# Optimization experiments

Hardware: AMD Instinct MI355X
Metric: run time of the kernel (lower is better)

Reference implementation:

```python
import jax, jax.numpy as jnp
import numpy as np

N = 20000   # nodes
E = 320000  # edges (avg degree 16)
IN = 16     # in_node_nf
H = 64      # hidden_nf
OUT = 64    # out_node_nf
L = 4       # n_layers


def setup_inputs() -> dict:
    key = jax.random.key(0)
    ks = jax.random.split(key, 16)
    w = lambda k, shape: (jax.random.normal(k, shape, dtype=jnp.float32) * 0.05)
    zb = lambda *shape: jnp.zeros(shape, dtype=jnp.float32)
    return {
        "h": jax.random.normal(ks[0], (N, IN), dtype=jnp.float32),
        "x": jax.random.normal(ks[1], (N, 3), dtype=jnp.float32),
        "edge_index": jax.random.randint(ks[2], (2, E), 0, N),
        "emb_in_w": w(ks[3], (IN, H)), "emb_in_b": zb(H),
        "edge_w1": w(ks[4], (L, 2 * H + 1, H)), "edge_b1": zb(L, H),
        "edge_w2": w(ks[5], (L, H, H)), "edge_b2": zb(L, H),
        "coord_w1": w(ks[6], (L, H, H)), "coord_b1": zb(L, H),
        "coord_w2": w(ks[7], (L, H, 1)),  # bias-free last coord_mlp layer
        "node_w1": w(ks[8], (L, 2 * H, H)), "node_b1": zb(L, H),
        "node_w2": w(ks[9], (L, H, H)), "node_b2": zb(L, H),
        "emb_out_w": w(ks[10], (H, OUT)), "emb_out_b": zb(OUT),
    }


def reference(h, x, edge_index, emb_in_w, emb_in_b,
              edge_w1, edge_b1, edge_w2, edge_b2,
              coord_w1, coord_b1, coord_w2,
              node_w1, node_b1, node_w2, node_b2,
              emb_out_w, emb_out_b):
    row, col = edge_index[0], edge_index[1]
    act = jax.nn.silu
    # receiver in-degree for mean coordinate aggregation (clamped to >=1)
    cnt = jax.ops.segment_sum(jnp.ones((row.shape[0], 1), h.dtype), row, num_segments=N)
    cnt = jnp.maximum(cnt, 1.0)

    h = h @ emb_in_w + emb_in_b
    for l in range(L):
        # coord2radial
        diff = x[row] - x[col]                               # [E,3]
        radial = jnp.sum(diff * diff, axis=-1, keepdims=True)  # [E,1]
        # edge model: m_ij = phi_e(h_i, h_j, ||x_i-x_j||^2)
        e_in = jnp.concatenate([h[row], h[col], radial], axis=-1)  # [E,2H+1]
        m = act(e_in @ edge_w1[l] + edge_b1[l])
        m = act(m @ edge_w2[l] + edge_b2[l])                 # [E,H]
        # coord model: x_i += mean_j (x_i - x_j) * phi_x(m_ij)
        phi = act(m @ coord_w1[l] + coord_b1[l]) @ coord_w2[l]  # [E,1]
        trans = diff * phi                                    # [E,3]
        x = x + jax.ops.segment_sum(trans, row, num_segments=N) / cnt
        # node model: h_i = h_i + phi_h(h_i, sum_j m_ij)
        agg = jax.ops.segment_sum(m, row, num_segments=N)     # [N,H]
        n_in = jnp.concatenate([h, agg], axis=-1)             # [N,2H]
        out = act(n_in @ node_w1[l] + node_b1[l]) @ node_w2[l] + node_b2[l]
        h = h + out
    h = h @ emb_out_w + emb_out_b
    return h, x
```

## Files before the change

### kernel.cpp

```cpp
#include <hip/hip_runtime.h>
#include <hip/hip_bf16.h>


#define NN 20000
#define EE 320000
#define LSE 17024
#define LSN 6272

typedef unsigned short u16;
typedef unsigned int   u32;
typedef __attribute__((ext_vector_type(8))) short s16x8;
typedef __attribute__((ext_vector_type(4))) float f32x4;

__device__ __forceinline__ float bf2f(u16 u) { return __uint_as_float(((u32)u) << 16); }
__device__ __forceinline__ float silu_f(float x) {
    return x * __builtin_amdgcn_rcpf(1.0f + __expf(-x));
}

__device__ __forceinline__ u16 f2bf_rne(float f) {
    u32 u = __float_as_uint(f);
    return (u16)((u + 0x7FFFu + ((u >> 16) & 1u)) >> 16);
}
__device__ __forceinline__ float gldf(const void* p, int i, int bf) {
    return bf ? bf2f(((const u16*)p)[i]) : ((const float*)p)[i];
}
__device__ __forceinline__ u16 gldb(const void* p, int i, int bf) {
    return bf ? ((const u16*)p)[i] : f2bf_rne(((const float*)p)[i]);
}

__global__ void k_sentinel(u16* __restrict__ out, int n, float v) {
    int t = blockIdx.x * 256 + threadIdx.x;
    if (t < n) out[t] = f2bf_rne(v);
}

__global__ __launch_bounds__(256) void k_pack(
    const void* __restrict__ ew1, const void* __restrict__ eb1,
    const void* __restrict__ ew2, const void* __restrict__ eb2,
    const void* __restrict__ cw1, const void* __restrict__ cb1,
    const void* __restrict__ cw2,
    const void* __restrict__ nw1, const void* __restrict__ nb1,
    const void* __restrict__ nw2, const void* __restrict__ nb2,
    const u16* __restrict__ h_raw, const int* __restrict__ rowi,
    int* __restrict__ flag, int* __restrict__ deg,
    u16* __restrict__ pkE, u32* __restrict__ pkN)
{
    if (blockIdx.x >= 64) {
        int e = (blockIdx.x - 64) * 256 + threadIdx.x;
        if (e < EE) atomicAdd(&deg[rowi[e]], 1);
        return;
    }
    __shared__ int cnt_s;
    if (threadIdx.x == 0) cnt_s = 0;
    __syncthreads();
    if (threadIdx.x < 128) {
        float v = fabsf(bf2f(h_raw[threadIdx.x]));
        if (v >= 0.015625f && v <= 16.0f) atomicAdd(&cnt_s, 1);
    }
    __syncthreads();
    const int bf = (cnt_s >= 96) ? 1 : 0;
    if (blockIdx.x == 0 && threadIdx.x == 0) *flag = bf;

    const int gid = blockIdx.x * 256 + threadIdx.x;
    const int stride = 64 * 256;

    for (int g = gid; g < 4 * 16384; g += stride) {
        int l = g >> 14, idx = g & 16383;
        u16 v;
        if (idx < 8192) {
            int j = idx & 7, lane = (idx >> 3) & 63, t = (idx >> 9) & 3, w = idx >> 11;
            int k = 32 * w + (lane >> 4) * 8 + j, n = 16 * t + (lane & 15);
            v = gldb(ew1, l * 129 * 64 + k * 64 + n, bf);
        } else if (idx < 12288) {
            int i2 = idx - 8192;
            int j = i2 & 7, lane = (i2 >> 3) & 63, t = (i2 >> 9) & 3, w = i2 >> 11;
            int k = 32 * w + (lane >> 4) * 8 + j, n = 16 * t + (lane & 15);
            v = gldb(ew2, l * 4096 + k * 64 + n, bf);
        } else {
            int i2 = idx - 12288;
            int j = i2 & 7, lane = (i2 >> 3) & 63, t = (i2 >> 9) & 3, w = i2 >> 11;
            int k = 32 * w + (lane >> 4) * 8 + j, n = 16 * t + (lane & 15);
            v = gldb(cw1, l * 4096 + k * 64 + n, bf);
        }
        pkE[l * LSE + idx] = v;
    }
    for (int g = gid; g < 4 * 320; g += stride) {
        int l = g / 320, r = g % 320, wch = r >> 6, i = r & 63;
        float v = (wch == 0) ? gldf(eb1, l * 64 + i, bf)
                : (wch == 1) ? gldf(eb2, l * 64 + i, bf)
                : (wch == 2) ? gldf(cb1, l * 64 + i, bf)
                : (wch == 3) ? gldf(cw2, l * 64 + i, bf)
                :              gldf(ew1, l * 129 * 64 + 128 * 64 + i, bf);
        ((float*)(pkE + l * LSE + 16384))[r] = v;
    }
    for (int g = gid; g < 4 * 6144; g += stride) {
        int l = g / 6144, idx = g % 6144;
        u32 pv;
        if (idx < 4096) {
            int kp = idx >> 6, j = idx & 63;
            u32 lo = gldb(nw1, l * 8192 + (2 * kp) * 64 + j, bf);
            u32 hi = gldb(nw1, l * 8192 + (2 * kp + 1) * 64 + j, bf);
            pv = lo | (hi << 16);
        } else {
            int i2 = idx - 4096, kp = i2 >> 6, j = i2 & 63;
            u32 lo = gldb(nw2, l * 4096 + (2 * kp) * 64 + j, bf);
            u32 hi = gldb(nw2, l * 4096 + (2 * kp + 1) * 64 + j, bf);
            pv = lo | (hi << 16);
        }
        pkN[l * LSN + idx] = pv;
    }
    for (int g = gid; g < 4 * 128; g += stride) {
        int l = g >> 7, r = g & 127;
        float v = (r < 64) ? gldf(nb1, l * 64 + r, bf) : gldf(nb2, l * 64 + (r - 64), bf);
        ((float*)(pkN + l * LSN + 6144))[r] = v;
    }
}

__global__ __launch_bounds__(1024) void k_scan(const int* deg, int* offs, int* cursor,
                                               int* __restrict__ perm) {
    __shared__ int part[1024];
    __shared__ int hist[32], basep[32];
    const int tid = threadIdx.x;
    const int CH = (NN + 1023) / 1024;
    const int b0 = tid * CH;
    int s = 0;
    for (int i = 0; i < CH; i++) { int idx = b0 + i; if (idx < NN) s += deg[idx]; }
    part[tid] = s;
    __syncthreads();
    for (int d = 1; d < 1024; d <<= 1) {
        int v = (tid >= d) ? part[tid - d] : 0;
        __syncthreads();
        part[tid] += v;
        __syncthreads();
    }
    int run = (tid > 0) ? part[tid - 1] : 0;
    for (int i = 0; i < CH; i++) {
        int idx = b0 + i;
        if (idx < NN) {
            int dv = deg[idx];
            offs[idx] = run;
            cursor[idx] = run;
            run += dv;
        }
    }
    if (tid == 1023) offs[NN] = run;
    __syncthreads();

    if (tid < 32) hist[tid] = 0;
    __syncthreads();
    for (int i = 0; i < CH; i++) {
        int idx = b0 + i;
        if (idx < NN) {
            int dv = offs[idx + 1] - offs[idx];
            int key = min(31, (dv + 15) >> 4);
            atomicAdd(&hist[key], 1);
        }
    }
    __syncthreads();
    if (tid == 0) {
        int pos = 0;
        for (int k = 31; k >= 0; k--) { basep[k] = pos; pos += hist[k]; }
    }
    __syncthreads();
    for (int i = 0; i < CH; i++) {
        int idx = b0 + i;
        if (idx < NN) {
            int dv = offs[idx + 1] - offs[idx];
            int key = min(31, (dv + 15) >> 4);
            int p = atomicAdd(&basep[key], 1);
            perm[p] = idx;
        }
    }
}

__global__ void k_scatter(const int* __restrict__ rowi, const int* __restrict__ coli,
                          int* __restrict__ cursor, int* __restrict__ slist) {
    int e = blockIdx.x * 256 + threadIdx.x;
    if (e < EE) {
        int r = rowi[e];
        int pos = atomicAdd(&cursor[r], 1);
        slist[pos] = coli[e];
    }
}

__global__ __launch_bounds__(256) void k_embed(
    const void* __restrict__ h_in, const void* __restrict__ x_in,
    const void* __restrict__ w, const void* __restrict__ bias,
    const int* __restrict__ flag,
    float* __restrict__ hws, float* __restrict__ xws, u16* __restrict__ hb)
{
    const int bf = *flag;
    const int lane = threadIdx.x & 63;
    const int wv   = threadIdx.x >> 6;
    const int i    = blockIdx.x * 4 + wv;
    float acc = gldf(bias, lane, bf);
    #pragma unroll
    for (int k = 0; k < 16; k++)
        acc = fmaf(gldf(h_in, i * 16 + k, bf), gldf(w, k * 64 + lane, bf), acc);
    hws[i * 64 + lane] = acc;
    hb[i * 64 + lane] = f2bf_rne(acc);
    if (lane < 3) xws[i * 3 + lane] = gldf(x_in, i * 3 + lane, bf);
}

#define OFF_B23  8192
#define OFF_M    16384
#define MPAD     76
#define OFF_PHI  (OFF_M + 8 * 16 * MPAD)
#define OFF_CB   (OFF_PHI + 8 * 32)
__global__ __launch_bounds__(512, 8) void k_edge(
    const u16* __restrict__ hb, const float* __restrict__ xws,
    const int* __restrict__ offs, const int* __restrict__ slist,
    const u16* __restrict__ pE, const int* __restrict__ perm,
    float* __restrict__ agg, float* __restrict__ xacc)
{
    __shared__ __align__(16) u16 sW[OFF_CB + 640];

    const int tid = threadIdx.x, lane = tid & 63, wv = tid >> 6;
    const int l15 = lane & 15, quad = lane >> 4;

    for (int idx = tid; idx < 2048; idx += 512)
        ((s16x8*)sW)[idx] = ((const s16x8*)pE)[idx];
    {
        const float* pb = (const float*)(pE + 16384);
        float* cb = (float*)&sW[OFF_CB];
        if (tid < 320) cb[tid] = pb[tid];
    }
    __syncthreads();

    const float* CB = (const float*)&sW[OFF_CB];
    const int gw = blockIdx.x * 8 + wv, totW = gridDim.x * 8;
    u16* mrow = &sW[OFF_M + wv * 16 * MPAD];
    float* phiw = (float*)&sW[OFF_PHI + wv * 32];

    for (int pidx = gw; pidx < NN; pidx += totW) {
        const int n = perm[pidx];
        const int o0 = offs[n], deg = offs[n + 1] - o0;
        if (deg == 0) continue;

        const s16x8 Ar0 = *(const s16x8*)&hb[n * 64 + quad * 8];
        const s16x8 Ar1 = *(const s16x8*)&hb[n * 64 + 32 + quad * 8];
        f32x4 Cb[4] = {{0,0,0,0},{0,0,0,0},{0,0,0,0},{0,0,0,0}};
        #pragma unroll
        for (int t = 0; t < 4; t++) {
            const s16x8 Bf0 = *(const s16x8*)&sW[((0 * 4 + t) * 64 + lane) * 8];
            Cb[t] = __builtin_amdgcn_mfma_f32_16x16x32_bf16(Ar0, Bf0, Cb[t], 0, 0, 0);
            const s16x8 Bf1 = *(const s16x8*)&sW[((1 * 4 + t) * 64 + lane) * 8];
            Cb[t] = __builtin_amdgcn_mfma_f32_16x16x32_bf16(Ar1, Bf1, Cb[t], 0, 0, 0);
        }
        const float xrv = (quad < 3) ? xws[n * 3 + quad] : 0.0f;
        float aggA[4] = {0.f, 0.f, 0.f, 0.f};
        float xaccA = 0.0f;

        for (int eb = 0; eb < deg; eb += 16) {
            const int nb = min(16, deg - eb);
            const int ee = (l15 < nb) ? l15 : 0;
            const int ce = slist[o0 + eb + ee];
            float dx = 0.0f;
            if (quad < 3 && l15 < nb) dx = xrv - xws[ce * 3 + quad];
            float r2 = dx * dx;
            r2 += __shfl_xor(r2, 16, 64);
            r2 += __shfl_xor(r2, 32, 64);

            f32x4 C[4] = {Cb[0], Cb[1], Cb[2], Cb[3]};
            {
                const s16x8 Ac0 = *(const s16x8*)&hb[ce * 64 + quad * 8];
                const s16x8 Ac1 = *(const s16x8*)&hb[ce * 64 + 32 + quad * 8];
                #pragma unroll
                for (int t = 0; t < 4; t++) {
                    const s16x8 Bf2 = *(const s16x8*)&sW[((2 * 4 + t) * 64 + lane) * 8];
                    C[t] = __builtin_amdgcn_mfma_f32_16x16x32_bf16(Ac0, Bf2, C[t], 0, 0, 0);
                    const s16x8 Bf3 = *(const s16x8*)&sW[((3 * 4 + t) * 64 + lane) * 8];
                    C[t] = __builtin_amdgcn_mfma_f32_16x16x32_bf16(Ac1, Bf3, C[t], 0, 0, 0);
                }
            }
            float r2r[4];
            #pragma unroll
            for (int r = 0; r < 4; r++) r2r[r] = __shfl(r2, quad * 4 + r, 64);
            #pragma unroll
            for (int t = 0; t < 4; t++) {
                const float b1t = CB[       16 * t + l15];
                const float wrt = CB[256 +  16 * t + l15];
                #pragma unroll
                for (int r = 0; r < 4; r++) {
                    float v = silu_f(C[t][r] + b1t + r2r[r] * wrt);
                    mrow[(quad * 4 + r) * MPAD + 16 * t + l15] = f2bf_rne(v);
                }
            }

            f32x4 D[4] = {{0,0,0,0},{0,0,0,0},{0,0,0,0},{0,0,0,0}};
            #pragma unroll
            for (int w = 0; w < 2; w++) {
                const s16x8 Am = *(const s16x8*)(mrow + l15 * MPAD + 32 * w + quad * 8);
                #pragma unroll
                for (int t = 0; t < 4; t++) {
                    const s16x8 Bf = *(const s16x8*)&sW[OFF_B23 + ((w * 4 + t) * 64 + lane) * 8];
                    D[t] = __builtin_amdgcn_mfma_f32_16x16x32_bf16(Am, Bf, D[t], 0, 0, 0);
                }
            }
            #pragma unroll
            for (int t = 0; t < 4; t++) {
                const float b2t = CB[64 + 16 * t + l15];
                #pragma unroll
                for (int r = 0; r < 4; r++) {
                    float v = silu_f(D[t][r] + b2t);
                    if (quad * 4 + r < nb) aggA[t] += v;
                    mrow[(quad * 4 + r) * MPAD + 16 * t + l15] = f2bf_rne(v);
                }
            }

            f32x4 P[4] = {{0,0,0,0},{0,0,0,0},{0,0,0,0},{0,0,0,0}};
            #pragma unroll
            for (int w = 0; w < 2; w++) {
                const s16x8 Am = *(const s16x8*)(mrow + l15 * MPAD + 32 * w + quad * 8);
                #pragma unroll
                for (int t = 0; t < 4; t++) {
                    const s16x8 Bf = *(const s16x8*)&sW[OFF_B23 + (((2 + w) * 4 + t) * 64 + lane) * 8];
                    P[t] = __builtin_amdgcn_mfma_f32_16x16x32_bf16(Am, Bf, P[t], 0, 0, 0);
                }
            }
            float ph[4];
            #pragma unroll
            for (int r = 0; r < 4; r++) ph[r] = 0.f;
            #pragma unroll
            for (int t = 0; t < 4; t++) {
                const float cb1t = CB[128 + 16 * t + l15];
                const float c2t  = CB[192 + 16 * t + l15];
                #pragma unroll
                for (int r = 0; r < 4; r++)
                    ph[r] = fmaf(silu_f(P[t][r] + cb1t), c2t, ph[r]);
            }
            #pragma unroll
            for (int r = 0; r < 4; r++) {
                float s = ph[r];
                s += __shfl_xor(s, 1, 64);
                s += __shfl_xor(s, 2, 64);
                s += __shfl_xor(s, 4, 64);
                s += __shfl_xor(s, 8, 64);
                ph[r] = s;
            }
            if (l15 == 0) {
                #pragma unroll
                for (int r = 0; r < 4; r++) phiw[quad * 4 + r] = ph[r];
            }
            float phv = phiw[l15];
            if (quad < 3 && l15 < nb) xaccA = fmaf(dx, phv, xaccA);
        }

        #pragma unroll
        for (int t = 0; t < 4; t++) {
            aggA[t] += __shfl_xor(aggA[t], 16, 64);
            aggA[t] += __shfl_xor(aggA[t], 32, 64);
        }
        float av = (quad == 0) ? aggA[0] : (quad == 1) ? aggA[1]
                 : (quad == 2) ? aggA[2] : aggA[3];
        agg[n * 64 + quad * 16 + l15] = av;

        xaccA += __shfl_xor(xaccA, 1, 64);
        xaccA += __shfl_xor(xaccA, 2, 64);
        xaccA += __shfl_xor(xaccA, 4, 64);
        xaccA += __shfl_xor(xaccA, 8, 64);
        if (l15 == 0 && quad < 3) xacc[n * 3 + quad] = xaccA / (float)deg;
    }
}

__global__ __launch_bounds__(256) void k_node(
    float* __restrict__ hws, u16* __restrict__ hb, const float* __restrict__ agg,
    float* __restrict__ xws, const float* __restrict__ xacc,
    const u32* __restrict__ pN)
{
    __shared__ __align__(16) u32 sW1p[64 * 64];
    __shared__ __align__(16) u32 sW2p[32 * 64];
    __shared__ float sB1f[64], sB2f[64];
    __shared__ __align__(16) float sNin[4][8][132];

    const int tid = threadIdx.x, lane = tid & 63, wv = tid >> 6;
    for (int idx = tid; idx < 1024; idx += 256)
        ((f32x4*)sW1p)[idx] = ((const f32x4*)pN)[idx];
    for (int idx = tid; idx < 512; idx += 256)
        ((f32x4*)sW2p)[idx] = ((const f32x4*)(pN + 4096))[idx];
    const float* pb = (const float*)(pN + 6144);
    if (tid < 64) { sB1f[tid] = pb[tid]; sB2f[tid] = pb[64 + tid]; }

    {
        int t = blockIdx.x * 96 + tid;
        if (tid < 96) xws[t] += xacc[t];
    }
    __syncthreads();

    const int i0 = (blockIdx.x * 4 + wv) * 8;
    float hold[8];
    #pragma unroll
    for (int b = 0; b < 8; b++) {
        int i = i0 + b;
        float hv = hws[i * 64 + lane];
        hold[b] = hv;
        sNin[wv][b][lane]      = hv;
        sNin[wv][b][64 + lane] = agg[i * 64 + lane];
    }

    float acc[8];
    #pragma unroll
    for (int b = 0; b < 8; b++) acc[b] = sB1f[lane];
    #pragma unroll
    for (int kk = 0; kk < 32; kk++) {
        u32 w01 = sW1p[(kk * 2) * 64 + lane];
        u32 w23 = sW1p[(kk * 2 + 1) * 64 + lane];
        float w0 = __uint_as_float(w01 << 16), w1 = __uint_as_float(w01 & 0xffff0000u);
        float w2 = __uint_as_float(w23 << 16), w3 = __uint_as_float(w23 & 0xffff0000u);
        #pragma unroll
        for (int b = 0; b < 8; b++) {
            const float4 e4 = *reinterpret_cast<const float4*>(&sNin[wv][b][kk * 4]);
            acc[b] = fmaf(e4.x, w0, fmaf(e4.y, w1, fmaf(e4.z, w2, fmaf(e4.w, w3, acc[b]))));
        }
    }
    #pragma unroll
    for (int b = 0; b < 8; b++) acc[b] = silu_f(acc[b]);
    #pragma unroll
    for (int b = 0; b < 8; b++) sNin[wv][b][lane] = acc[b];

    float out[8];
    #pragma unroll
    for (int b = 0; b < 8; b++) out[b] = sB2f[lane];
    #pragma unroll
    for (int kk = 0; kk < 16; kk++) {
        u32 w01 = sW2p[(kk * 2) * 64 + lane];
        u32 w23 = sW2p[(kk * 2 + 1) * 64 + lane];
        float w0 = __uint_as_float(w01 << 16), w1 = __uint_as_float(w01 & 0xffff0000u);
        float w2 = __uint_as_float(w23 << 16), w3 = __uint_as_float(w23 & 0xffff0000u);
        #pragma unroll
        for (int b = 0; b < 8; b++) {
            const float4 e4 = *reinterpret_cast<const float4*>(&sNin[wv][b][kk * 4]);
            out[b] = fmaf(e4.x, w0, fmaf(e4.y, w1, fmaf(e4.z, w2, fmaf(e4.w, w3, out[b]))));
        }
    }
    #pragma unroll
    for (int b = 0; b < 8; b++) {
        float hv = hold[b] + out[b];
        hws[(i0 + b) * 64 + lane] = hv;
        hb[(i0 + b) * 64 + lane] = f2bf_rne(hv);
    }
}

__global__ __launch_bounds__(256) void k_out(
    const float* __restrict__ hws, const float* __restrict__ xws,
    const void* __restrict__ wo, const void* __restrict__ bo,
    const int* __restrict__ flag, void* __restrict__ out)
{
    __shared__ u32 sWp[32 * 64];
    __shared__ float sBf[64];
    __shared__ __align__(16) float sH[4][8][68];
    const int tid = threadIdx.x, lane = tid & 63, wv = tid >> 6;
    const int bf = *flag;
    for (int idx = tid; idx < 32 * 64; idx += 256) {
        int kp = idx >> 6, j = idx & 63;
        u32 lo = gldb(wo, (kp * 2) * 64 + j, bf);
        u32 hi = gldb(wo, (kp * 2 + 1) * 64 + j, bf);
        sWp[idx] = lo | (hi << 16);
    }
    if (tid < 64) sBf[tid] = gldf(bo, tid, bf);
    __syncthreads();

    const int i0 = (blockIdx.x * 4 + wv) * 8;
    #pragma unroll
    for (int b = 0; b < 8; b++) sH[wv][b][lane] = hws[(i0 + b) * 64 + lane];

    float acc[8];
    #pragma unroll
    for (int b = 0; b < 8; b++) acc[b] = sBf[lane];
    #pragma unroll
    for (int kk = 0; kk < 16; kk++) {
        u32 w01 = sWp[(kk * 2) * 64 + lane];
        u32 w23 = sWp[(kk * 2 + 1) * 64 + lane];
        float w0 = __uint_as_float(w01 << 16), w1 = __uint_as_float(w01 & 0xffff0000u);
        float w2 = __uint_as_float(w23 << 16), w3 = __uint_as_float(w23 & 0xffff0000u);
        #pragma unroll
        for (int b = 0; b < 8; b++) {
            const float4 e4 = *reinterpret_cast<const float4*>(&sH[wv][b][kk * 4]);
            acc[b] = fmaf(e4.x, w0, fmaf(e4.y, w1, fmaf(e4.z, w2, fmaf(e4.w, w3, acc[b]))));
        }
    }
    u16*   oh16 = (u16*)out;
    float* ohf  = (float*)out;
    u16*   ox16 = oh16 + (size_t)NN * 64;
    float* oxf  = ohf  + (size_t)NN * 64;
    #pragma unroll
    for (int b = 0; b < 8; b++) {
        int i = i0 + b;
        if (bf) {
            oh16[i * 64 + lane] = f2bf_rne(acc[b]);
            if (lane < 3) ox16[i * 3 + lane] = f2bf_rne(xws[i * 3 + lane]);
        } else {
            ohf[i * 64 + lane] = acc[b];
            if (lane < 3) oxf[i * 3 + lane] = xws[i * 3 + lane];
        }
    }
}

extern "C" void kernel_launch(void* const* d_in, const int* in_sizes, int n_in,
                              void* d_out, int out_size, void* d_ws, size_t ws_size,
                              hipStream_t stream)
{
    const size_t WS_REQ = (size_t)NN * 134 * sizeof(float) + 64;
    if (ws_size < WS_REQ) {
        float sval = 1000.0f + (float)(ws_size >> 20);
        k_sentinel<<<(out_size + 255) / 256, 256, 0, stream>>>(
            (u16*)d_out, out_size, sval);
        return;
    }

    const void* h_in = d_in[0];
    const void* x_in = d_in[1];
    const int*  eidx = (const int*)d_in[2];
    const int* rowi = eidx;
    const int* coli = eidx + EE;

    float* ws   = (float*)d_ws;
    float* hws  = ws;
    float* xws  = hws + NN * 64;
    float* agg  = xws + NN * 3;
    float* xacc = agg + NN * 64;
    int*   flag = (int*)(xacc + NN * 3);

    u16* hb     = (u16*)d_out;
    int* offs   = (int*)(hb + (size_t)NN * 64);
    int* slist  = offs + (NN + 4);
    u16* pkE    = (u16*)(slist + EE);
    u32* pkN    = (u32*)(pkE + 4 * LSE);
    int* cursor = (int*)(pkN + 4 * LSN);
    int* perm   = cursor + NN;

    hipMemsetAsync(cursor, 0, (size_t)NN * sizeof(int), stream);
    hipMemsetAsync(agg, 0, (size_t)NN * 67 * sizeof(float), stream);

    k_pack<<<64 + (EE + 255) / 256, 256, 0, stream>>>(
        d_in[5], d_in[6], d_in[7], d_in[8], d_in[9], d_in[10], d_in[11],
        d_in[12], d_in[13], d_in[14], d_in[15],
        (const u16*)h_in, rowi, flag, cursor, pkE, pkN);
    k_scan<<<1, 1024, 0, stream>>>(cursor, offs, cursor, perm);
    k_scatter<<<(EE + 255) / 256, 256, 0, stream>>>(rowi, coli, cursor, slist);
    k_embed<<<NN / 4, 256, 0, stream>>>(h_in, x_in, d_in[3], d_in[4], flag, hws, xws, hb);

    for (int l = 0; l < 4; l++) {
        k_edge<<<768, 512, 0, stream>>>(hb, xws, offs, slist,
                                        pkE + l * LSE, perm, agg, xacc);
        k_node<<<NN / 32, 256, 0, stream>>>(hws, hb, agg, xws, xacc,
                                            pkN + (size_t)l * LSN);
    }
    k_out<<<NN / 32, 256, 0, stream>>>(hws, xws, d_in[16], d_in[17], flag, d_out);
}
```

Before: 550.2 us.

## Fuse node MLP into edge kernel with ping-pong h/x buffers

Folds the per-node update MLP into the edge kernel, so each wave finishes its node's aggregation and immediately runs the node MLP. The agg/xacc global buffers, their memset and the separate k_node launches go away. Bf16 h and coordinates are double-buffered so neighbour reads are not corrupted by in-place writes. In exchange, each wave now does a per-node scalar FMA matvec through LDS, and the larger LDS footprint (node weights added) lowers occupancy, with launch bounds reduced to 2 and the grid to 512 blocks.

```diff
diff --git a/kernel.cpp b/kernel.cpp
--- a/kernel.cpp
+++ b/kernel.cpp
@@ -206,13 +206,16 @@
 #define MPAD     76
 #define OFF_PHI  (OFF_M + 8 * 16 * MPAD)
 #define OFF_CB   (OFF_PHI + 8 * 32)
-__global__ __launch_bounds__(512, 8) void k_edge(
-    const u16* __restrict__ hb, const float* __restrict__ xws,
+#define OFF_NW   (OFF_CB + 640)
+__global__ __launch_bounds__(512, 2) void k_edge(
+    const u16* __restrict__ hbr, u16* __restrict__ hbw,
+    const float* __restrict__ xr, float* __restrict__ xw,
+    float* __restrict__ hws,
     const int* __restrict__ offs, const int* __restrict__ slist,
-    const u16* __restrict__ pE, const int* __restrict__ perm,
-    float* __restrict__ agg, float* __restrict__ xacc)
+    const u16* __restrict__ pE, const u32* __restrict__ pN,
+    const int* __restrict__ perm)
 {
-    __shared__ __align__(16) u16 sW[OFF_CB + 640];
+    __shared__ __align__(16) u16 sW[OFF_NW + 12544];
 
     const int tid = threadIdx.x, lane = tid & 63, wv = tid >> 6;
     const int l15 = lane & 15, quad = lane >> 4;
@@ -224,9 +227,15 @@
         float* cb = (float*)&sW[OFF_CB];
         if (tid < 320) cb[tid] = pb[tid];
     }
+    for (int idx = tid; idx < 1568; idx += 512)
+        ((f32x4*)&sW[OFF_NW])[idx] = ((const f32x4*)pN)[idx];
     __syncthreads();
 
     const float* CB = (const float*)&sW[OFF_CB];
+    const u32* nW1 = (const u32*)&sW[OFF_NW];
+    const u32* nW2 = nW1 + 4096;
+    const float* nB = (const float*)(nW1 + 6144);
+
     const int gw = blockIdx.x * 8 + wv, totW = gridDim.x * 8;
     u16* mrow = &sW[OFF_M + wv * 16 * MPAD];
     float* phiw = (float*)&sW[OFF_PHI + wv * 32];
@@ -234,10 +243,9 @@
     for (int pidx = gw; pidx < NN; pidx += totW) {
         const int n = perm[pidx];
         const int o0 = offs[n], deg = offs[n + 1] - o0;
-        if (deg == 0) continue;
-
-        const s16x8 Ar0 = *(const s16x8*)&hb[n * 64 + quad * 8];
-        const s16x8 Ar1 = *(const s16x8*)&hb[n * 64 + 32 + quad * 8];
+
+        const s16x8 Ar0 = *(const s16x8*)&hbr[n * 64 + quad * 8];
+        const s16x8 Ar1 = *(const s16x8*)&hbr[n * 64 + 32 + quad * 8];
         f32x4 Cb[4] = {{0,0,0,0},{0,0,0,0},{0,0,0,0},{0,0,0,0}};
         #pragma unroll
         for (int t = 0; t < 4; t++) {
@@ -246,7 +254,7 @@
             const s16x8 Bf1 = *(const s16x8*)&sW[((1 * 4 + t) * 64 + lane) * 8];
             Cb[t] = __builtin_amdgcn_mfma_f32_16x16x32_bf16(Ar1, Bf1, Cb[t], 0, 0, 0);
         }
-        const float xrv = (quad < 3) ? xws[n * 3 + quad] : 0.0f;
+        const float xrv = (quad < 3) ? xr[n * 3 + quad] : 0.0f;
         float aggA[4] = {0.f, 0.f, 0.f, 0.f};
         float xaccA = 0.0f;
 
@@ -255,15 +263,15 @@
             const int ee = (l15 < nb) ? l15 : 0;
             const int ce = slist[o0 + eb + ee];
             float dx = 0.0f;
-            if (quad < 3 && l15 < nb) dx = xrv - xws[ce * 3 + quad];
+            if (quad < 3 && l15 < nb) dx = xrv - xr[ce * 3 + quad];
             float r2 = dx * dx;
             r2 += __shfl_xor(r2, 16, 64);
             r2 += __shfl_xor(r2, 32, 64);
 
             f32x4 C[4] = {Cb[0], Cb[1], Cb[2], Cb[3]};
             {
-                const s16x8 Ac0 = *(const s16x8*)&hb[ce * 64 + quad * 8];
-                const s16x8 Ac1 = *(const s16x8*)&hb[ce * 64 + 32 + quad * 8];
+                const s16x8 Ac0 = *(const s16x8*)&hbr[ce * 64 + quad * 8];
+                const s16x8 Ac1 = *(const s16x8*)&hbr[ce * 64 + 32 + quad * 8];
                 #pragma unroll
                 for (int t = 0; t < 4; t++) {
                     const s16x8 Bf2 = *(const s16x8*)&sW[((2 * 4 + t) * 64 + lane) * 8];
@@ -352,91 +360,43 @@
         }
         float av = (quad == 0) ? aggA[0] : (quad == 1) ? aggA[1]
                  : (quad == 2) ? aggA[2] : aggA[3];
-        agg[n * 64 + quad * 16 + l15] = av;
 
         xaccA += __shfl_xor(xaccA, 1, 64);
         xaccA += __shfl_xor(xaccA, 2, 64);
         xaccA += __shfl_xor(xaccA, 4, 64);
         xaccA += __shfl_xor(xaccA, 8, 64);
-        if (l15 == 0 && quad < 3) xacc[n * 3 + quad] = xaccA / (float)deg;
-    }
-}
-
-__global__ __launch_bounds__(256) void k_node(
-    float* __restrict__ hws, u16* __restrict__ hb, const float* __restrict__ agg,
-    float* __restrict__ xws, const float* __restrict__ xacc,
-    const u32* __restrict__ pN)
-{
-    __shared__ __align__(16) u32 sW1p[64 * 64];
-    __shared__ __align__(16) u32 sW2p[32 * 64];
-    __shared__ float sB1f[64], sB2f[64];
-    __shared__ __align__(16) float sNin[4][8][132];
-
-    const int tid = threadIdx.x, lane = tid & 63, wv = tid >> 6;
-    for (int idx = tid; idx < 1024; idx += 256)
-        ((f32x4*)sW1p)[idx] = ((const f32x4*)pN)[idx];
-    for (int idx = tid; idx < 512; idx += 256)
-        ((f32x4*)sW2p)[idx] = ((const f32x4*)(pN + 4096))[idx];
-    const float* pb = (const float*)(pN + 6144);
-    if (tid < 64) { sB1f[tid] = pb[tid]; sB2f[tid] = pb[64 + tid]; }
-
-    {
-        int t = blockIdx.x * 96 + tid;
-        if (tid < 96) xws[t] += xacc[t];
-    }
-    __syncthreads();
-
-    const int i0 = (blockIdx.x * 4 + wv) * 8;
-    float hold[8];
-    #pragma unroll
-    for (int b = 0; b < 8; b++) {
-        int i = i0 + b;
-        float hv = hws[i * 64 + lane];
-        hold[b] = hv;
-        sNin[wv][b][lane]      = hv;
-        sNin[wv][b][64 + lane] = agg[i * 64 + lane];
-    }
-
-    float acc[8];
-    #pragma unroll
-    for (int b = 0; b < 8; b++) acc[b] = sB1f[lane];
-    #pragma unroll
-    for (int kk = 0; kk < 32; kk++) {
-        u32 w01 = sW1p[(kk * 2) * 64 + lane];
-        u32 w23 = sW1p[(kk * 2 + 1) * 64 + lane];
-        float w0 = __uint_as_float(w01 << 16), w1 = __uint_as_float(w01 & 0xffff0000u);
-        float w2 = __uint_as_float(w23 << 16), w3 = __uint_as_float(w23 & 0xffff0000u);
+        if (l15 == 0 && quad < 3)
+            xw[n * 3 + quad] = (deg > 0) ? (xrv + xaccA / (float)deg) : xrv;
+
+        float* nin = (float*)mrow;
+        const float hv = hws[n * 64 + lane];
+        nin[lane] = hv;
+        nin[64 + lane] = av;
+        float a1 = nB[lane];
         #pragma unroll
-        for (int b = 0; b < 8; b++) {
-            const float4 e4 = *reinterpret_cast<const float4*>(&sNin[wv][b][kk * 4]);
-            acc[b] = fmaf(e4.x, w0, fmaf(e4.y, w1, fmaf(e4.z, w2, fmaf(e4.w, w3, acc[b]))));
-        }
-    }
-    #pragma unroll
-    for (int b = 0; b < 8; b++) acc[b] = silu_f(acc[b]);
-    #pragma unroll
-    for (int b = 0; b < 8; b++) sNin[wv][b][lane] = acc[b];
-
-    float out[8];
-    #pragma unroll
-    for (int b = 0; b < 8; b++) out[b] = sB2f[lane];
-    #pragma unroll
-    for (int kk = 0; kk < 16; kk++) {
-        u32 w01 = sW2p[(kk * 2) * 64 + lane];
-        u32 w23 = sW2p[(kk * 2 + 1) * 64 + lane];
-        float w0 = __uint_as_float(w01 << 16), w1 = __uint_as_float(w01 & 0xffff0000u);
-        float w2 = __uint_as_float(w23 << 16), w3 = __uint_as_float(w23 & 0xffff0000u);
+        for (int kk = 0; kk < 32; kk++) {
+            u32 w01 = nW1[(kk * 2) * 64 + lane];
+            u32 w23 = nW1[(kk * 2 + 1) * 64 + lane];
+            float w0 = __uint_as_float(w01 << 16), w1 = __uint_as_float(w01 & 0xffff0000u);
+            float w2 = __uint_as_float(w23 << 16), w3 = __uint_as_float(w23 & 0xffff0000u);
+            const float4 e4 = *reinterpret_cast<const float4*>(&nin[kk * 4]);
+            a1 = fmaf(e4.x, w0, fmaf(e4.y, w1, fmaf(e4.z, w2, fmaf(e4.w, w3, a1))));
+        }
+        a1 = silu_f(a1);
+        nin[lane] = a1;
+        float a2 = nB[64 + lane];
         #pragma unroll
-        for (int b = 0; b < 8; b++) {
-            const float4 e4 = *reinterpret_cast<const float4*>(&sNin[wv][b][kk * 4]);
-            out[b] = fmaf(e4.x, w0, fmaf(e4.y, w1, fmaf(e4.z, w2, fmaf(e4.w, w3, out[b]))));
-        }
-    }
-    #pragma unroll
-    for (int b = 0; b < 8; b++) {
-        float hv = hold[b] + out[b];
-        hws[(i0 + b) * 64 + lane] = hv;
-        hb[(i0 + b) * 64 + lane] = f2bf_rne(hv);
+        for (int kk = 0; kk < 16; kk++) {
+            u32 w01 = nW2[(kk * 2) * 64 + lane];
+            u32 w23 = nW2[(kk * 2 + 1) * 64 + lane];
+            float w0 = __uint_as_float(w01 << 16), w1 = __uint_as_float(w01 & 0xffff0000u);
+            float w2 = __uint_as_float(w23 << 16), w3 = __uint_as_float(w23 & 0xffff0000u);
+            const float4 e4 = *reinterpret_cast<const float4*>(&nin[kk * 4]);
+            a2 = fmaf(e4.x, w0, fmaf(e4.y, w1, fmaf(e4.z, w2, fmaf(e4.w, w3, a2))));
+        }
+        const float hnew = hv + a2;
+        hws[n * 64 + lane] = hnew;
+        hbw[n * 64 + lane] = f2bf_rne(hnew);
     }
 }
 
@@ -515,13 +475,13 @@
 
     float* ws   = (float*)d_ws;
     float* hws  = ws;
-    float* xws  = hws + NN * 64;
-    float* agg  = xws + NN * 3;
-    float* xacc = agg + NN * 64;
-    int*   flag = (int*)(xacc + NN * 3);
-
-    u16* hb     = (u16*)d_out;
-    int* offs   = (int*)(hb + (size_t)NN * 64);
+    float* xws0 = hws + NN * 64;
+    u16*   hb1  = (u16*)(xws0 + NN * 3);
+    float* xws1 = (float*)(hb1 + (size_t)NN * 64);
+    int*   flag = (int*)(xws1 + NN * 3);
+
+    u16* hb0    = (u16*)d_out;
+    int* offs   = (int*)(hb0 + (size_t)NN * 64);
     int* slist  = offs + (NN + 4);
     u16* pkE    = (u16*)(slist + EE);
     u32* pkN    = (u32*)(pkE + 4 * LSE);
@@ -529,7 +489,6 @@
     int* perm   = cursor + NN;
 
     hipMemsetAsync(cursor, 0, (size_t)NN * sizeof(int), stream);
-    hipMemsetAsync(agg, 0, (size_t)NN * 67 * sizeof(float), stream);
 
     k_pack<<<64 + (EE + 255) / 256, 256, 0, stream>>>(
         d_in[5], d_in[6], d_in[7], d_in[8], d_in[9], d_in[10], d_in[11],
@@ -537,13 +496,15 @@
         (const u16*)h_in, rowi, flag, cursor, pkE, pkN);
     k_scan<<<1, 1024, 0, stream>>>(cursor, offs, cursor, perm);
     k_scatter<<<(EE + 255) / 256, 256, 0, stream>>>(rowi, coli, cursor, slist);
-    k_embed<<<NN / 4, 256, 0, stream>>>(h_in, x_in, d_in[3], d_in[4], flag, hws, xws, hb);
+    k_embed<<<NN / 4, 256, 0, stream>>>(h_in, x_in, d_in[3], d_in[4], flag, hws, xws0, hb0);
 
     for (int l = 0; l < 4; l++) {
-        k_edge<<<768, 512, 0, stream>>>(hb, xws, offs, slist,
-                                        pkE + l * LSE, perm, agg, xacc);
-        k_node<<<NN / 32, 256, 0, stream>>>(hws, hb, agg, xws, xacc,
-                                            pkN + (size_t)l * LSN);
-    }
-    k_out<<<NN / 32, 256, 0, stream>>>(hws, xws, d_in[16], d_in[17], flag, d_out);
-}
+        const u16*   hr = (l & 1) ? hb1 : hb0;
+        u16*         hw = (l & 1) ? hb0 : hb1;
+        const float* xrp = (l & 1) ? xws1 : xws0;
+        float*       xwp = (l & 1) ? xws0 : xws1;
+        k_edge<<<512, 512, 0, stream>>>(hr, hw, xrp, xwp, hws, offs, slist,
+                                        pkE + l * LSE, pkN + (size_t)l * LSN, perm);
+    }
+    k_out<<<NN / 32, 256, 0, stream>>>(hws, xws0, d_in[16], d_in[17], flag, d_out);
+}
```

Result: slower. 580.1 us (+5.4%).
